# Performance work log

Measured on AMD Instinct MI355X. Metric: run time of the kernel, lower is better.

## Reference

```python
import jax, jax.numpy as jnp
import numpy as np

N_NODES = 10000
IN_CH = 512
HID = 128
HEADS = 4
OUT_CH = 256
N_EDGES = 160000
NEG_SLOPE = 0.2  # PyG GATConv default


def gat_conv(x, src, dst, W, a_src, a_dst, b):
    """PyG-style GATConv. x:[N,F_in], W:[F_in,H*C], a_src/a_dst:[H,C], b:[H*C].
    src/dst already include self-loops. Returns [N, H*C] (concat heads)."""
    N = x.shape[0]
    H, C = a_src.shape
    h = (x @ W).reshape(N, H, C)                     # [N,H,C]
    e_src = jnp.einsum('nhc,hc->nh', h, a_src)        # [N,H]
    e_dst = jnp.einsum('nhc,hc->nh', h, a_dst)
    alpha = jax.nn.leaky_relu(e_src[src] + e_dst[dst], NEG_SLOPE)  # [E,H]
    # softmax over incoming edges of each destination node
    m = jax.ops.segment_max(alpha, dst, num_segments=N)            # [N,H]
    ex = jnp.exp(alpha - m[dst])
    denom = jax.ops.segment_sum(ex, dst, num_segments=N)           # [N,H]
    coeff = ex / (denom[dst] + 1e-16)                              # [E,H]
    out = jax.ops.segment_sum(coeff[:, :, None] * h[src], dst, num_segments=N)  # [N,H,C]
    return out.reshape(N, H * C) + b


def _edges_with_self_loops(edge_index, n):
    loops = jnp.arange(n, dtype=edge_index.dtype)
    src = jnp.concatenate([edge_index[0], loops])
    dst = jnp.concatenate([edge_index[1], loops])
    return src, dst


def setup_inputs() -> dict:
    key = jax.random.key(0)
    ks = jax.random.split(key, 20)
    s = 0.05
    inp = {
        'x': jax.random.normal(ks[0], (N_NODES, IN_CH), jnp.float32),
        'W1': jax.random.normal(ks[1], (IN_CH, HEADS * HID), jnp.float32) * s,
        'a1s': jax.random.normal(ks[2], (HEADS, HID), jnp.float32) * s,
        'a1d': jax.random.normal(ks[3], (HEADS, HID), jnp.float32) * s,
        'b1': jnp.zeros((HEADS * HID,), jnp.float32),
        'W2': jax.random.normal(ks[4], (HEADS * HID, HEADS * HID), jnp.float32) * s,
        'a2s': jax.random.normal(ks[5], (HEADS, HID), jnp.float32) * s,
        'a2d': jax.random.normal(ks[6], (HEADS, HID), jnp.float32) * s,
        'b2': jnp.zeros((HEADS * HID,), jnp.float32),
        'W3': jax.random.normal(ks[7], (HEADS * HID, HID), jnp.float32) * s,
        'a3s': jax.random.normal(ks[8], (1, HID), jnp.float32) * s,
        'a3d': jax.random.normal(ks[9], (1, HID), jnp.float32) * s,
        'b3': jnp.zeros((HID,), jnp.float32),
        'Wl': jax.random.normal(ks[10], (HID, OUT_CH), jnp.float32) * s,
        'bl': jnp.zeros((OUT_CH,), jnp.float32),
        'Wr': jax.random.normal(ks[11], (IN_CH, OUT_CH), jnp.float32) * s,
        'br': jnp.zeros((OUT_CH,), jnp.float32),
        'edge_index': jax.random.randint(ks[12], (2, N_EDGES), 0, N_NODES, jnp.int64 if jax.config.jax_enable_x64 else jnp.int32),
    }
    return inp


def reference(x, W1, a1s, a1d, b1, W2, a2s, a2d, b2, W3, a3s, a3d, b3, Wl, bl, Wr, br, edge_index):
    src, dst = _edges_with_self_loops(edge_index, x.shape[0])
    residual = x @ Wr + br
    h = jax.nn.elu(gat_conv(x, src, dst, W1, a1s, a1d, b1))
    h = jax.nn.elu(gat_conv(h, src, dst, W2, a2s, a2d, b2))
    h = jax.nn.elu(gat_conv(h, src, dst, W3, a3s, a3d, b3))
    return h @ Wl + bl + residual
```

## Files before the change

kernel.cpp:

```cpp
#include <hip/hip_runtime.h>
#include <hip/hip_bf16.h>
#include <cstdint>
#include <cstddef>

#define N_NODES 10000
#define M_PAD   10240
#define HEADS   4

typedef __bf16 bfrag8 __attribute__((ext_vector_type(8)));
typedef __bf16 bfrag2 __attribute__((ext_vector_type(2)));
typedef float  floatx4 __attribute__((ext_vector_type(4)));
typedef float  floatx2 __attribute__((ext_vector_type(2)));

#define S0V (M_PAD * 512 / 8)
#define S1E (512 * 512 / 8)
#define S2E (512 * 512 / 8)
#define S3E (512 * 128 / 8)
#define S4E (128 * 256 / 8)
#define S5E (512 * 256 / 8)

__global__ __launch_bounds__(256) void prep(const float* __restrict__ x,
                                            const float* __restrict__ W1,
                                            const float* __restrict__ W2,
                                            const float* __restrict__ W3,
                                            const float* __restrict__ Wl,
                                            const float* __restrict__ Wr,
                                            const int* __restrict__ edst, int E,
                                            __bf16* __restrict__ xb,
                                            __bf16* __restrict__ W1T,
                                            __bf16* __restrict__ W2T,
                                            __bf16* __restrict__ W3T,
                                            __bf16* __restrict__ WlT,
                                            __bf16* __restrict__ WrT,
                                            int* __restrict__ deg) {
    int i = blockIdx.x * 256 + threadIdx.x;
    if (i < S0V) {
        int base = i * 8;
        int row = base >> 9;
        bfrag8 r = {};
        if (row < N_NODES) {
            float4 f0 = ((const float4*)x)[i * 2];
            float4 f1 = ((const float4*)x)[i * 2 + 1];
            r[0] = (__bf16)f0.x; r[1] = (__bf16)f0.y; r[2] = (__bf16)f0.z; r[3] = (__bf16)f0.w;
            r[4] = (__bf16)f1.x; r[5] = (__bf16)f1.y; r[6] = (__bf16)f1.z; r[7] = (__bf16)f1.w;
        }
        *(bfrag8*)(xb + base) = r;
    } else if ((i -= S0V) < S1E) {
        int n = i & 511, kb = (i >> 9) * 8;
        bfrag8 r;
#pragma unroll
        for (int t = 0; t < 8; ++t) r[t] = (__bf16)W1[(kb + t) * 512 + n];
        *(bfrag8*)(W1T + n * 512 + kb) = r;
    } else if ((i -= S1E) < S2E) {
        int n = i & 511, kb = (i >> 9) * 8;
        bfrag8 r;
#pragma unroll
        for (int t = 0; t < 8; ++t) r[t] = (__bf16)W2[(kb + t) * 512 + n];
        *(bfrag8*)(W2T + n * 512 + kb) = r;
    } else if ((i -= S2E) < S3E) {
        int n = i & 127, kb = (i >> 7) * 8;
        bfrag8 r;
#pragma unroll
        for (int t = 0; t < 8; ++t) r[t] = (__bf16)W3[(kb + t) * 128 + n];
        *(bfrag8*)(W3T + n * 512 + kb) = r;
    } else if ((i -= S3E) < S4E) {
        int n = i & 255, kb = (i >> 8) * 8;
        bfrag8 r;
#pragma unroll
        for (int t = 0; t < 8; ++t) r[t] = (__bf16)Wl[(kb + t) * 256 + n];
        *(bfrag8*)(WlT + n * 128 + kb) = r;
    } else if ((i -= S4E) < S5E) {
        int n = i & 255, kb = (i >> 8) * 8;
        bfrag8 r;
#pragma unroll
        for (int t = 0; t < 8; ++t) r[t] = (__bf16)Wr[(kb + t) * 256 + n];
        *(bfrag8*)(WrT + n * 512 + kb) = r;
    } else if ((i -= S5E) < E) {
        atomicAdd(&deg[edst[i]], 1);
    }
}


__global__ __launch_bounds__(256) void scan_kernel(const int* __restrict__ deg,
                                                   int* __restrict__ rowptr,
                                                   int* __restrict__ cursor, int n) {
    __shared__ int wtot[4], woff[4];
    int t = threadIdx.x, lane = t & 63, wv = t >> 6;
    int chunk = (n + 255) / 256;
    int beg = t * chunk, end = beg + chunk; if (end > n) end = n; if (beg > n) beg = n;
    int s = 0;
    for (int i = beg; i < end; ++i) s += deg[i] + 1;
    int v = s;
#pragma unroll
    for (int off = 1; off < 64; off <<= 1) {
        int o = __shfl_up(v, off);
        if (lane >= off) v += o;
    }
    if (lane == 63) wtot[wv] = v;
    __syncthreads();
    if (t == 0) {
        int r = 0;
#pragma unroll
        for (int i = 0; i < 4; ++i) { woff[i] = r; r += wtot[i]; }
        rowptr[n] = r;
    }
    __syncthreads();
    int off = woff[wv] + v - s;
    for (int i = beg; i < end; ++i) {
        rowptr[i] = off; cursor[i] = off;
        off += deg[i] + 1;
    }
}

__global__ __launch_bounds__(256) void scatter_kernel(const int* __restrict__ src,
                                                      const int* __restrict__ dst, int E, int n,
                                                      int* __restrict__ cursor,
                                                      int* __restrict__ csr) {
    int i = blockIdx.x * 256 + threadIdx.x;
    if (i < E) {
        int pos = atomicAdd(&cursor[dst[i]], 1);
        csr[pos] = src[i];
    } else if (i < E + n) {
        int v = i - E;
        int pos = atomicAdd(&cursor[v], 1);
        csr[pos] = v;
    }
}


template <int NT>
__device__ __forceinline__ void gemm_loop(const __bf16* __restrict__ A,
                                          const __bf16* __restrict__ BT, int K,
                                          int m0, int n0, int wave, int lane,
                                          __bf16* As, __bf16* Bs,
                                          floatx4 (&acc)[2][NT]) {
    int r = wave * 8 + (lane >> 3);
    int kof = (lane & 7) * 8;
    const __bf16* gA = A + (size_t)(m0 + r) * K + kof;
    const __bf16* gB = BT + (size_t)(n0 + r) * K + kof;
    __bf16* lA = As + r * 64 + kof;
    __bf16* lB = Bs + r * 64 + kof;
    const __bf16* fA = As + (wave * 32 + (lane & 15)) * 64 + (lane >> 4) * 8;
    const __bf16* fB = Bs + (lane & 15) * 64 + (lane >> 4) * 8;

    for (int k0 = 0; k0 < K; k0 += 64) {
#pragma unroll
        for (int u = 0; u < 4; ++u)
            __builtin_amdgcn_global_load_lds(
                (const __attribute__((address_space(1))) void*)(gA + (size_t)u * 32 * K),
                (__attribute__((address_space(3))) void*)(lA + u * 32 * 64), 16, 0, 0);
#pragma unroll
        for (int u = 0; u < NT / 2; ++u)
            __builtin_amdgcn_global_load_lds(
                (const __attribute__((address_space(1))) void*)(gB + (size_t)u * 32 * K),
                (__attribute__((address_space(3))) void*)(lB + u * 32 * 64), 16, 0, 0);
        gA += 64; gB += 64;
        __syncthreads();

#pragma unroll
        for (int ks = 0; ks < 2; ++ks) {
            bfrag8 a0 = *(const bfrag8*)(fA + ks * 32);
            bfrag8 a1 = *(const bfrag8*)(fA + 16 * 64 + ks * 32);
#pragma unroll
            for (int nt = 0; nt < NT; ++nt) {
                bfrag8 b = *(const bfrag8*)(fB + nt * 16 * 64 + ks * 32);
                acc[0][nt] = __builtin_amdgcn_mfma_f32_16x16x32_bf16(a0, b, acc[0][nt], 0, 0, 0);
                acc[1][nt] = __builtin_amdgcn_mfma_f32_16x16x32_bf16(a1, b, acc[1][nt], 0, 0, 0);
            }
        }
        __syncthreads();
    }
}

__global__ __launch_bounds__(256) void gemm_h(const __bf16* __restrict__ A,
                                              const __bf16* __restrict__ BT,
                                              unsigned char* __restrict__ C8,
                                              int N, int K, int H,
                                              const float* __restrict__ as_,
                                              const float* __restrict__ ad_,
                                              float* __restrict__ esp,
                                              float* __restrict__ edp) {
    __shared__ __align__(16) __bf16 As[128 * 64];
    __shared__ __align__(16) __bf16 Bs[64 * 64];
    int tid = threadIdx.x, wave = tid >> 6, lane = tid & 63;
    int m0 = blockIdx.x * 128, n0 = blockIdx.y * 64;
    floatx4 acc[2][4] = {};
    gemm_loop<4>(A, BT, K, m0, n0, wave, lane, As, Bs, acc);

    int crow = m0 + wave * 32 + (lane >> 4) * 4;
    int ccol = n0 + (lane & 15);
#pragma unroll
    for (int mt = 0; mt < 2; ++mt)
#pragma unroll
        for (int nt = 0; nt < 4; ++nt)
#pragma unroll
            for (int r = 0; r < 4; ++r) {
                float v = acc[mt][nt][r];
                size_t o = (size_t)(crow + mt * 16 + r) * N + ccol + nt * 16;
                int p = __builtin_amdgcn_cvt_pk_fp8_f32(v, v, 0, false);
                C8[o] = (unsigned char)(p & 0xff);
            }

    int head = n0 >> 7;
    int half = (n0 >> 6) & 1;
    float a_sv[4], a_dv[4];
#pragma unroll
    for (int nt = 0; nt < 4; ++nt) {
        int cin = (n0 & 64) + nt * 16 + (lane & 15);
        a_sv[nt] = as_[head * 128 + cin];
        a_dv[nt] = ad_[head * 128 + cin];
    }
    float* ep = esp + (size_t)half * M_PAD * H;
    float* dp = edp + (size_t)half * M_PAD * H;
#pragma unroll
    for (int mt = 0; mt < 2; ++mt)
#pragma unroll
        for (int r = 0; r < 4; ++r) {
            float ps = 0.f, pd = 0.f;
#pragma unroll
            for (int nt = 0; nt < 4; ++nt) {
                float v = acc[mt][nt][r];
                ps += v * a_sv[nt];
                pd += v * a_dv[nt];
            }
#pragma unroll
            for (int off = 8; off; off >>= 1) {
                ps += __shfl_xor(ps, off);
                pd += __shfl_xor(pd, off);
            }
            if ((lane & 15) == 0) {
                int row = crow + mt * 16 + r;
                ep[row * H + head] = ps;
                dp[row * H + head] = pd;
            }
        }
}

__global__ __launch_bounds__(256) void gemm_final(const __bf16* __restrict__ A1,
                                                  const __bf16* __restrict__ B1T, int K1,
                                                  const __bf16* __restrict__ A2,
                                                  const __bf16* __restrict__ B2T, int K2,
                                                  float* __restrict__ C,
                                                  const float* __restrict__ bias1,
                                                  const float* __restrict__ bias2,
                                                  int M, int N) {
    __shared__ __align__(16) __bf16 As[128 * 64];
    __shared__ __align__(16) __bf16 Bs[64 * 64];
    int tid = threadIdx.x, wave = tid >> 6, lane = tid & 63;
    int m0 = blockIdx.x * 128, n0 = blockIdx.y * 64;
    floatx4 acc[2][4] = {};
    gemm_loop<4>(A1, B1T, K1, m0, n0, wave, lane, As, Bs, acc);
    gemm_loop<4>(A2, B2T, K2, m0, n0, wave, lane, As, Bs, acc);

    int crow = m0 + wave * 32 + (lane >> 4) * 4;
    int ccol = n0 + (lane & 15);
#pragma unroll
    for (int mt = 0; mt < 2; ++mt)
#pragma unroll
        for (int nt = 0; nt < 4; ++nt)
#pragma unroll
            for (int r = 0; r < 4; ++r) {
                int row = crow + mt * 16 + r;
                int col = ccol + nt * 16;
                if (row < M)
                    C[(size_t)row * N + col] = acc[mt][nt][r] + bias1[col] + bias2[col];
            }
}


template <int H>
__global__ __launch_bounds__(256) void gather_agg(const unsigned char* __restrict__ H8,
                                                  const float* __restrict__ esp,
                                                  const float* __restrict__ edp,
                                                  const int* __restrict__ rowptr,
                                                  const int* __restrict__ csr,
                                                  const float* __restrict__ bias,
                                                  __bf16* __restrict__ outb) {
    constexpr int F = H * 128;
    constexpr int CH = F / 64;
    constexpr int PO = M_PAD * H;
    int wave = threadIdx.x >> 6, lane = threadIdx.x & 63;
    int node = blockIdx.x * 4 + wave;
    if (node >= M_PAD) return;
    int hsel = (H == 4) ? (lane >> 4) : 0;
    __bf16* op = outb + (size_t)node * F + lane * CH;
    if (node >= N_NODES) {
        if (H == 4) { bfrag8 z = {}; *(bfrag8*)op = z; }
        else        { bfrag2 z = {}; *(bfrag2*)op = z; }
        return;
    }
    const unsigned char* hp = H8 + lane * CH;
    float edv = edp[node * H + hsel] + edp[PO + node * H + hsel];
    int beg = rowptr[node], end = rowptr[node + 1];
    float acc[CH] = {};
    float wsum = 0.f;
    int j = beg;
    for (; j + 7 < end; j += 8) {
        int s[8];
        float e[8];
#pragma unroll
        for (int u = 0; u < 8; ++u) s[u] = csr[j + u];
#pragma unroll
        for (int u = 0; u < 8; ++u)
            e[u] = esp[s[u] * H + hsel] + esp[PO + s[u] * H + hsel];
        if (H == 4) {
            uint2 p[8];
#pragma unroll
            for (int u = 0; u < 8; ++u) p[u] = *(const uint2*)(hp + (size_t)s[u] * F);
#pragma unroll
            for (int u = 0; u < 8; ++u) {
                float t = e[u] + edv;
                t = t > 0.f ? t : 0.2f * t;
                float wgt = __expf(t);
                wsum += wgt;
                floatx2 f0 = __builtin_amdgcn_cvt_pk_f32_fp8(p[u].x, false);
                floatx2 f1 = __builtin_amdgcn_cvt_pk_f32_fp8(p[u].x, true);
                floatx2 f2 = __builtin_amdgcn_cvt_pk_f32_fp8(p[u].y, false);
                floatx2 f3 = __builtin_amdgcn_cvt_pk_f32_fp8(p[u].y, true);
                acc[0] += wgt * f0[0]; acc[1] += wgt * f0[1];
                acc[2] += wgt * f1[0]; acc[3] += wgt * f1[1];
                acc[4] += wgt * f2[0]; acc[5] += wgt * f2[1];
                acc[6] += wgt * f3[0]; acc[7] += wgt * f3[1];
            }
        } else {
            unsigned short p[8];
#pragma unroll
            for (int u = 0; u < 8; ++u) p[u] = *(const unsigned short*)(hp + (size_t)s[u] * F);
#pragma unroll
            for (int u = 0; u < 8; ++u) {
                float t = e[u] + edv;
                t = t > 0.f ? t : 0.2f * t;
                float wgt = __expf(t);
                wsum += wgt;
                floatx2 f0 = __builtin_amdgcn_cvt_pk_f32_fp8((int)p[u], false);
                acc[0] += wgt * f0[0]; acc[1] += wgt * f0[1];
            }
        }
    }
    for (; j < end; ++j) {
        int s0 = csr[j];
        float t = esp[s0 * H + hsel] + esp[PO + s0 * H + hsel] + edv;
        t = t > 0.f ? t : 0.2f * t;
        float wgt = __expf(t);
        wsum += wgt;
        if (H == 4) {
            uint2 p = *(const uint2*)(hp + (size_t)s0 * F);
            floatx2 f0 = __builtin_amdgcn_cvt_pk_f32_fp8(p.x, false);
            floatx2 f1 = __builtin_amdgcn_cvt_pk_f32_fp8(p.x, true);
            floatx2 f2 = __builtin_amdgcn_cvt_pk_f32_fp8(p.y, false);
            floatx2 f3 = __builtin_amdgcn_cvt_pk_f32_fp8(p.y, true);
            acc[0] += wgt * f0[0]; acc[1] += wgt * f0[1];
            acc[2] += wgt * f1[0]; acc[3] += wgt * f1[1];
            acc[4] += wgt * f2[0]; acc[5] += wgt * f2[1];
            acc[6] += wgt * f3[0]; acc[7] += wgt * f3[1];
        } else {
            unsigned short p = *(const unsigned short*)(hp + (size_t)s0 * F);
            floatx2 f0 = __builtin_amdgcn_cvt_pk_f32_fp8((int)p, false);
            acc[0] += wgt * f0[0]; acc[1] += wgt * f0[1];
        }
    }
    float inv = 1.f / (wsum + 1e-16f);
    if (H == 4) {
        bfrag8 r;
#pragma unroll
        for (int k = 0; k < 8; ++k) {
            float o = acc[k] * inv + bias[lane * 8 + k];
            o = o > 0.f ? o : __expf(o) - 1.f;
            r[k] = (__bf16)o;
        }
        *(bfrag8*)op = r;
    } else {
        bfrag2 r;
#pragma unroll
        for (int k = 0; k < 2; ++k) {
            float o = acc[k] * inv + bias[lane * 2 + k];
            o = o > 0.f ? o : __expf(o) - 1.f;
            r[k] = (__bf16)o;
        }
        *(bfrag2*)op = r;
    }
}


extern "C" void kernel_launch(void* const* d_in, const int* in_sizes, int n_in,
                              void* d_out, int out_size, void* d_ws, size_t ws_size,
                              hipStream_t stream) {
    const float* x   = (const float*)d_in[0];
    const float* W1  = (const float*)d_in[1];
    const float* a1s = (const float*)d_in[2];
    const float* a1d = (const float*)d_in[3];
    const float* b1  = (const float*)d_in[4];
    const float* W2  = (const float*)d_in[5];
    const float* a2s = (const float*)d_in[6];
    const float* a2d = (const float*)d_in[7];
    const float* b2  = (const float*)d_in[8];
    const float* W3  = (const float*)d_in[9];
    const float* a3s = (const float*)d_in[10];
    const float* a3d = (const float*)d_in[11];
    const float* b3  = (const float*)d_in[12];
    const float* Wl  = (const float*)d_in[13];
    const float* bl  = (const float*)d_in[14];
    const float* Wr  = (const float*)d_in[15];
    const float* br  = (const float*)d_in[16];
    const int*   ei  = (const int*)d_in[17];
    const int E = in_sizes[17] / 2;
    const int* esrc = ei;
    const int* edst = ei + E;
    const int slots = E + N_NODES;
    float* out = (float*)d_out;

    char* w = (char*)d_ws;
    auto alloc = [&](size_t b) { char* p = w; w += (b + 255) & ~(size_t)255; return p; };
    __bf16* xb  = (__bf16*)alloc((size_t)M_PAD * 512 * 2);
    __bf16* hb  = (__bf16*)alloc((size_t)M_PAD * 512 * 2);
    __bf16* hb3 = (__bf16*)alloc((size_t)M_PAD * 128 * 2);
    unsigned char* Hi8 = (unsigned char*)alloc((size_t)M_PAD * 512);
    __bf16* W1T = (__bf16*)alloc(512 * 512 * 2);
    __bf16* W2T = (__bf16*)alloc(512 * 512 * 2);
    __bf16* W3T = (__bf16*)alloc(128 * 512 * 2);
    __bf16* WlT = (__bf16*)alloc(256 * 128 * 2);
    __bf16* WrT = (__bf16*)alloc(256 * 512 * 2);
    float* esp    = (float*)alloc((size_t)2 * M_PAD * HEADS * 4);
    float* edp    = (float*)alloc((size_t)2 * M_PAD * HEADS * 4);
    int*   deg    = (int*)alloc(N_NODES * 4);
    int*   rowptr = (int*)alloc((N_NODES + 1) * 4);
    int*   cursor = (int*)alloc(N_NODES * 4);
    int*   csr    = (int*)alloc((size_t)slots * 4);

    (void)hipMemsetAsync(deg, 0, N_NODES * sizeof(int), stream);

    const int sp_total = S0V + S1E + S2E + S3E + S4E + S5E + E;
    prep<<<(sp_total + 255) / 256, 256, 0, stream>>>(x, W1, W2, W3, Wl, Wr, edst, E,
                                                     xb, W1T, W2T, W3T, WlT, WrT, deg);
    scan_kernel<<<1, 256, 0, stream>>>(deg, rowptr, cursor, N_NODES);
    scatter_kernel<<<(E + N_NODES + 255) / 256, 256, 0, stream>>>(esrc, edst, E, N_NODES,
                                                                  cursor, csr);

    gemm_h<<<dim3(M_PAD / 128, 8), 256, 0, stream>>>(xb, W1T, Hi8, 512, 512, 4,
                                                     a1s, a1d, esp, edp);
    gather_agg<4><<<M_PAD / 4, 256, 0, stream>>>(Hi8, esp, edp, rowptr, csr, b1, hb);
    gemm_h<<<dim3(M_PAD / 128, 8), 256, 0, stream>>>(hb, W2T, Hi8, 512, 512, 4,
                                                     a2s, a2d, esp, edp);
    gather_agg<4><<<M_PAD / 4, 256, 0, stream>>>(Hi8, esp, edp, rowptr, csr, b2, hb);
    gemm_h<<<dim3(M_PAD / 128, 2), 256, 0, stream>>>(hb, W3T, Hi8, 128, 512, 1,
                                                     a3s, a3d, esp, edp);
    gather_agg<1><<<M_PAD / 4, 256, 0, stream>>>(Hi8, esp, edp, rowptr, csr, b3, hb3);
    gemm_final<<<dim3(M_PAD / 128, 4), 256, 0, stream>>>(xb, WrT, 512, hb3, WlT, 128,
                                                         out, br, bl, N_NODES, 256);
}
```

Before: 260.7 us.

## Software-pipeline edge gathers and interleave split attention scores as float2

Rewrites the gather-aggregate loop to prefetch the next chunk of 8 edges (indices, scores, fp8 features) while the current chunk is computed. The scalar tail loop is replaced by padded chunks whose out-of-range lanes get zero weight. The GEMM epilogue now stores the two half-head partial attention scores interleaved, so one float2 load replaces two strided loads. This doubles the gather registers per thread, which may lower occupancy, and adds redundant loads on padded edges.

```diff
diff --git a/kernel.cpp b/kernel.cpp
--- a/kernel.cpp
+++ b/kernel.cpp
@@ -210,8 +210,6 @@
         a_sv[nt] = as_[head * 128 + cin];
         a_dv[nt] = ad_[head * 128 + cin];
     }
-    float* ep = esp + (size_t)half * M_PAD * H;
-    float* dp = edp + (size_t)half * M_PAD * H;
 #pragma unroll
     for (int mt = 0; mt < 2; ++mt)
 #pragma unroll
@@ -230,8 +228,8 @@
             }
             if ((lane & 15) == 0) {
                 int row = crow + mt * 16 + r;
-                ep[row * H + head] = ps;
-                dp[row * H + head] = pd;
+                esp[(size_t)(row * H + head) * 2 + half] = ps;
+                edp[(size_t)(row * H + head) * 2 + half] = pd;
             }
         }
 }
@@ -278,7 +276,6 @@
                                                   __bf16* __restrict__ outb) {
     constexpr int F = H * 128;
     constexpr int CH = F / 64;
-    constexpr int PO = M_PAD * H;
     int wave = threadIdx.x >> 6, lane = threadIdx.x & 63;
     int node = blockIdx.x * 4 + wave;
     if (node >= M_PAD) return;
@@ -290,75 +287,93 @@
         return;
     }
     const unsigned char* hp = H8 + lane * CH;
-    float edv = edp[node * H + hsel] + edp[PO + node * H + hsel];
+    const float2* es2 = (const float2*)esp;
+    float2 dv = ((const float2*)edp)[node * H + hsel];
+    float edv = dv.x + dv.y;
     int beg = rowptr[node], end = rowptr[node + 1];
+    int nch = (end - beg + 7) >> 3;
     float acc[CH] = {};
     float wsum = 0.f;
     int j = beg;
-    for (; j + 7 < end; j += 8) {
-        int s[8];
-        float e[8];
-#pragma unroll
-        for (int u = 0; u < 8; ++u) s[u] = csr[j + u];
-#pragma unroll
-        for (int u = 0; u < 8; ++u)
-            e[u] = esp[s[u] * H + hsel] + esp[PO + s[u] * H + hsel];
-        if (H == 4) {
-            uint2 p[8];
-#pragma unroll
-            for (int u = 0; u < 8; ++u) p[u] = *(const uint2*)(hp + (size_t)s[u] * F);
+
+    if constexpr (H == 4) {
+        int s0[8]; float2 e0[8]; uint2 p0[8];
+#pragma unroll
+        for (int u = 0; u < 8; ++u) s0[u] = csr[(j + u < end) ? j + u : end - 1];
+#pragma unroll
+        for (int u = 0; u < 8; ++u) e0[u] = es2[s0[u] * H + hsel];
+#pragma unroll
+        for (int u = 0; u < 8; ++u) p0[u] = *(const uint2*)(hp + (size_t)s0[u] * F);
+        for (int c = 0; c < nch; ++c) {
+            int s1[8]; float2 e1[8]; uint2 p1[8];
+            int jn = j + 8;
+            bool more = (c + 1 < nch);
+            if (more) {
+#pragma unroll
+                for (int u = 0; u < 8; ++u) s1[u] = csr[(jn + u < end) ? jn + u : end - 1];
+#pragma unroll
+                for (int u = 0; u < 8; ++u) e1[u] = es2[s1[u] * H + hsel];
+#pragma unroll
+                for (int u = 0; u < 8; ++u) p1[u] = *(const uint2*)(hp + (size_t)s1[u] * F);
+            }
 #pragma unroll
             for (int u = 0; u < 8; ++u) {
-                float t = e[u] + edv;
+                float t = e0[u].x + e0[u].y + edv;
                 t = t > 0.f ? t : 0.2f * t;
-                float wgt = __expf(t);
+                float wgt = (j + u < end) ? __expf(t) : 0.f;
                 wsum += wgt;
-                floatx2 f0 = __builtin_amdgcn_cvt_pk_f32_fp8(p[u].x, false);
-                floatx2 f1 = __builtin_amdgcn_cvt_pk_f32_fp8(p[u].x, true);
-                floatx2 f2 = __builtin_amdgcn_cvt_pk_f32_fp8(p[u].y, false);
-                floatx2 f3 = __builtin_amdgcn_cvt_pk_f32_fp8(p[u].y, true);
+                floatx2 f0 = __builtin_amdgcn_cvt_pk_f32_fp8(p0[u].x, false);
+                floatx2 f1 = __builtin_amdgcn_cvt_pk_f32_fp8(p0[u].x, true);
+                floatx2 f2 = __builtin_amdgcn_cvt_pk_f32_fp8(p0[u].y, false);
+                floatx2 f3 = __builtin_amdgcn_cvt_pk_f32_fp8(p0[u].y, true);
                 acc[0] += wgt * f0[0]; acc[1] += wgt * f0[1];
                 acc[2] += wgt * f1[0]; acc[3] += wgt * f1[1];
                 acc[4] += wgt * f2[0]; acc[5] += wgt * f2[1];
                 acc[6] += wgt * f3[0]; acc[7] += wgt * f3[1];
             }
-        } else {
-            unsigned short p[8];
-#pragma unroll
-            for (int u = 0; u < 8; ++u) p[u] = *(const unsigned short*)(hp + (size_t)s[u] * F);
+            if (more) {
+#pragma unroll
+                for (int u = 0; u < 8; ++u) { s0[u] = s1[u]; e0[u] = e1[u]; p0[u] = p1[u]; }
+            }
+            j = jn;
+        }
+    } else {
+        int s0[8]; float2 e0[8]; unsigned short p0[8];
+#pragma unroll
+        for (int u = 0; u < 8; ++u) s0[u] = csr[(j + u < end) ? j + u : end - 1];
+#pragma unroll
+        for (int u = 0; u < 8; ++u) e0[u] = es2[s0[u] * H + hsel];
+#pragma unroll
+        for (int u = 0; u < 8; ++u) p0[u] = *(const unsigned short*)(hp + (size_t)s0[u] * F);
+        for (int c = 0; c < nch; ++c) {
+            int s1[8]; float2 e1[8]; unsigned short p1[8];
+            int jn = j + 8;
+            bool more = (c + 1 < nch);
+            if (more) {
+#pragma unroll
+                for (int u = 0; u < 8; ++u) s1[u] = csr[(jn + u < end) ? jn + u : end - 1];
+#pragma unroll
+                for (int u = 0; u < 8; ++u) e1[u] = es2[s1[u] * H + hsel];
+#pragma unroll
+                for (int u = 0; u < 8; ++u) p1[u] = *(const unsigned short*)(hp + (size_t)s1[u] * F);
+            }
 #pragma unroll
             for (int u = 0; u < 8; ++u) {
-                float t = e[u] + edv;
+                float t = e0[u].x + e0[u].y + edv;
                 t = t > 0.f ? t : 0.2f * t;
-                float wgt = __expf(t);
+                float wgt = (j + u < end) ? __expf(t) : 0.f;
                 wsum += wgt;
-                floatx2 f0 = __builtin_amdgcn_cvt_pk_f32_fp8((int)p[u], false);
+                floatx2 f0 = __builtin_amdgcn_cvt_pk_f32_fp8((int)p0[u], false);
                 acc[0] += wgt * f0[0]; acc[1] += wgt * f0[1];
             }
-        }
-    }
-    for (; j < end; ++j) {
-        int s0 = csr[j];
-        float t = esp[s0 * H + hsel] + esp[PO + s0 * H + hsel] + edv;
-        t = t > 0.f ? t : 0.2f * t;
-        float wgt = __expf(t);
-        wsum += wgt;
-        if (H == 4) {
-            uint2 p = *(const uint2*)(hp + (size_t)s0 * F);
-            floatx2 f0 = __builtin_amdgcn_cvt_pk_f32_fp8(p.x, false);
-            floatx2 f1 = __builtin_amdgcn_cvt_pk_f32_fp8(p.x, true);
-            floatx2 f2 = __builtin_amdgcn_cvt_pk_f32_fp8(p.y, false);
-            floatx2 f3 = __builtin_amdgcn_cvt_pk_f32_fp8(p.y, true);
-            acc[0] += wgt * f0[0]; acc[1] += wgt * f0[1];
-            acc[2] += wgt * f1[0]; acc[3] += wgt * f1[1];
-            acc[4] += wgt * f2[0]; acc[5] += wgt * f2[1];
-            acc[6] += wgt * f3[0]; acc[7] += wgt * f3[1];
-        } else {
-            unsigned short p = *(const unsigned short*)(hp + (size_t)s0 * F);
-            floatx2 f0 = __builtin_amdgcn_cvt_pk_f32_fp8((int)p, false);
-            acc[0] += wgt * f0[0]; acc[1] += wgt * f0[1];
-        }
-    }
+            if (more) {
+#pragma unroll
+                for (int u = 0; u < 8; ++u) { s0[u] = s1[u]; e0[u] = e1[u]; p0[u] = p1[u]; }
+            }
+            j = jn;
+        }
+    }
+
     float inv = 1.f / (wsum + 1e-16f);
     if (H == 4) {
         bfrag8 r;
```

After: 276.4 us. 1.06x slower.
